# Kernel tuning notes

Measured on AMD Instinct MI355X. Metric: run time of the kernel, lower is better.

Reference implementation:

```python
import jax, jax.numpy as jnp
import numpy as np

WS = (7, 7, 7)          # window size (S, H, W)
NUM_HEADS = 6
DIM = 192
B_, NW = 128, 32        # total windows, windows per image (mask dim)
N = WS[0] * WS[1] * WS[2]  # 343 tokens per window


def _relative_position_index():
    # Faithful replica of the torch __init__ logic (incl. indexing='xy' and
    # the 3*W1-1 / 2*W1-1 multipliers).
    cs = np.arange(WS[0]); ch = np.arange(WS[1]); cw = np.arange(WS[2])
    coords = np.stack(np.meshgrid(cs, ch, cw, indexing='xy'))  # (3, Wh, Ws, Ww)
    cf = coords.reshape(3, -1)                                  # (3, N)
    rel = cf[:, :, None] - cf[:, None, :]                       # (3, N, N)
    rel = rel.transpose(1, 2, 0).astype(np.int64)               # (N, N, 3)
    rel[:, :, 0] += WS[0] - 1
    rel[:, :, 1] += WS[1] - 1
    rel[:, :, 2] += WS[2] - 1
    rel[:, :, 0] *= 3 * WS[1] - 1
    rel[:, :, 1] *= 2 * WS[1] - 1
    return rel.sum(-1)                                          # (N, N) int


def setup_inputs() -> dict:
    key = jax.random.key(0)
    ks = jax.random.split(key, 6)
    C = DIM
    x = jax.random.normal(ks[0], (B_, N, C), dtype=jnp.float32)
    mask = jax.random.normal(ks[1], (NW, N, N), dtype=jnp.float32)
    qkv_w = jax.random.normal(ks[2], (3 * C, C), dtype=jnp.float32) * 0.02
    qkv_b = jnp.zeros((3 * C,), dtype=jnp.float32)
    proj_w = jax.random.normal(ks[3], (C, C), dtype=jnp.float32) * 0.02
    proj_b = jnp.zeros((C,), dtype=jnp.float32)
    table_len = (2 * WS[0] - 1) * (2 * WS[1] - 1) * (2 * WS[2] - 1)
    rpb_table = jax.random.normal(ks[4], (table_len, NUM_HEADS), dtype=jnp.float32) * 0.02
    rel_index = jnp.asarray(_relative_position_index(), dtype=jnp.int32)
    return {"x": x, "mask": mask, "qkv_w": qkv_w, "qkv_b": qkv_b,
            "proj_w": proj_w, "proj_b": proj_b, "rpb_table": rpb_table,
            "rel_index": rel_index}


def reference(x, mask, qkv_w, qkv_b, proj_w, proj_b, rpb_table, rel_index):
    B, n, C = x.shape
    H = NUM_HEADS
    hd = C // H
    scale = hd ** (-0.5)
    qkv = x @ qkv_w.T + qkv_b                      # (B, N, 3C)
    qkv = qkv.reshape(B, n, 3, H, hd).transpose(2, 0, 3, 1, 4)  # (3, B, H, N, hd)
    q, k, v = qkv[0] * scale, qkv[1], qkv[2]
    attn = jnp.einsum('bhnd,bhmd->bhnm', q, k)     # (B, H, N, N)
    bias = rpb_table[rel_index.reshape(-1)].reshape(n, n, H)
    attn = attn + bias.transpose(2, 0, 1)[None]    # (B, H, N, N)
    nW = mask.shape[0]
    attn = attn.reshape(B // nW, nW, H, n, n) + mask[None, :, None]
    attn = jax.nn.softmax(attn.reshape(B, H, n, n), axis=-1)
    out = jnp.einsum('bhnm,bhmd->bhnd', attn, v)   # (B, H, N, hd)
    out = out.transpose(0, 2, 1, 3).reshape(B, n, C)
    return out @ proj_w.T + proj_b
```

## Files before the change

### kernel.cpp

```cpp
#include <hip/hip_runtime.h>
#include <hip/hip_fp16.h>
#include <hip/hip_bf16.h>
#include <stdint.h>

#define WN 343
#define NH 6
#define HD 32
#define CD 192
#define NB 128
#define NWM 32
#define BMROW 352
#define BMSLICE (11*16*BMROW)

typedef __attribute__((ext_vector_type(8))) short short8;
typedef __attribute__((ext_vector_type(4))) float f32x4;

__device__ __forceinline__ unsigned short f2bf(float f) {
  union { float f; uint32_t u; } v; v.f = f;
  uint32_t r = v.u + 0x7fffu + ((v.u >> 16) & 1u);
  return (unsigned short)(r >> 16);
}

__device__ __forceinline__ uint32_t pk2bf(float a, float b) {
  __hip_bfloat162 h = __float22bfloat162_rn(make_float2(a, b));
  return *(uint32_t*)&h;
}

__global__ __launch_bounds__(256) void prep_kernel(
    const float* __restrict__ wq, const float* __restrict__ wp,
    unsigned short* __restrict__ wqb, unsigned short* __restrict__ wpb,
    const int* __restrict__ rel, const float* __restrict__ rpb,
    const float* __restrict__ mask, uint32_t* __restrict__ bP,
    uint32_t* __restrict__ mP) {
  __shared__ float M[352][33];
  const int bid = blockIdx.x;
  if (bid < 66 + 352) {
    const bool isBias = (bid < 66);
    const int sub = isBias ? bid : bid - 66;
    const int grp = sub / 11;
    const int kc = sub - grp * 11;
    const int k0 = kc * 32;
    const float* mw = mask + (size_t)grp * (WN * WN);
    for (int idx = threadIdx.x; idx < 352 * 32; idx += 256) {
      int n = idx >> 5, k = idx & 31;
      float v;
      if (isBias) {
        int nc = (n < WN) ? n : (WN - 1);
        v = (k0 + k < WN) ? rpb[rel[nc * WN + k0 + k] * NH + grp] : -60000.0f;
      } else {
        v = (n < WN && k0 + k < WN) ? mw[n * WN + k0 + k] : 0.0f;
      }
      M[n][k] = v;
    }
    __syncthreads();
    uint32_t* outp = (isBias ? bP : mP) + (size_t)grp * BMSLICE + kc * 16 * BMROW;
#pragma unroll
    for (int rr = 0; rr < 16; ++rr) {
      int kkA = (rr >> 2) * 8 + (rr & 3);
#pragma unroll
      for (int j = 0; j < 2; ++j) {
        int n = threadIdx.x + 256 * j;
        if (n < 352) {
          __half2 hv; hv.x = __float2half(M[n][kkA]); hv.y = __float2half(M[n][kkA + 4]);
          outp[rr * BMROW + n] = *(uint32_t*)&hv;
        }
      }
    }
    return;
  }
  const int NWQ = 3 * CD * CD;
  const int NWP = CD * CD;
  int i4 = ((bid - 418) * 256 + threadIdx.x) * 4;
  const float* src; unsigned short* dst; int off;
  if (i4 < NWQ) { src = wq; dst = wqb; off = i4; }
  else if (i4 < NWQ + NWP) { src = wp; dst = wpb; off = i4 - NWQ; }
  else return;
  f32x4 v = *(const f32x4*)(src + off);
  union { uint2 u2; uint32_t d[2]; } o;
  o.d[0] = pk2bf(v[0], v[1]);
  o.d[1] = pk2bf(v[2], v[3]);
  *(uint2*)(dst + off) = o.u2;
}

__global__ __launch_bounds__(256) void qkv_kernel(
    const float* __restrict__ x, const unsigned short* __restrict__ wqb,
    const float* __restrict__ bvec,
    unsigned short* __restrict__ qb, unsigned short* __restrict__ kb,
    unsigned short* __restrict__ vb) {
  __shared__ __align__(16) unsigned short Xs[128][40];
  __shared__ __align__(16) unsigned short Ws[192][40];
  const int tid = threadIdx.x;
  const int wave = tid >> 6, lane = tid & 63;
  const int quad = lane >> 4, c = lane & 15;
  const int m0 = blockIdx.x * 128;
  const int s = blockIdx.y;
  const int n0 = s * 192;

  f32x4 acc[2][12];
#pragma unroll
  for (int i = 0; i < 2; ++i)
#pragma unroll
    for (int j = 0; j < 12; ++j) acc[i][j] = (f32x4){0.f, 0.f, 0.f, 0.f};

  for (int kt = 0; kt < 6; ++kt) {
    const int k0 = kt * 32;
#pragma unroll
    for (int it = 0; it < 2; ++it) {
      int tq = tid + it * 256;
      int r = tq >> 2, ch = tq & 3;
      const float* src = x + (size_t)(m0 + r) * CD + k0 + ch * 8;
      f32x4 a = *(const f32x4*)src;
      f32x4 b = *(const f32x4*)(src + 4);
      union { short8 v8; uint32_t d[4]; } pk;
      pk.d[0] = pk2bf(a[0], a[1]);
      pk.d[1] = pk2bf(a[2], a[3]);
      pk.d[2] = pk2bf(b[0], b[1]);
      pk.d[3] = pk2bf(b[2], b[3]);
      *(short8*)&Xs[r][ch * 8] = pk.v8;
    }
#pragma unroll
    for (int it = 0; it < 3; ++it) {
      int r = it * 64 + (tid >> 2), ch = tid & 3;
      *(short8*)&Ws[r][ch * 8] =
          *(const short8*)(wqb + (size_t)(n0 + r) * CD + k0 + ch * 8);
    }
    __syncthreads();
    short8 af0 = *(const short8*)&Xs[wave * 32 + c][quad * 8];
    short8 af1 = *(const short8*)&Xs[wave * 32 + 16 + c][quad * 8];
#pragma unroll
    for (int j = 0; j < 12; ++j) {
      short8 bfr = *(const short8*)&Ws[j * 16 + c][quad * 8];
      acc[0][j] = __builtin_amdgcn_mfma_f32_16x16x32_bf16(af0, bfr, acc[0][j], 0, 0, 0);
      acc[1][j] = __builtin_amdgcn_mfma_f32_16x16x32_bf16(af1, bfr, acc[1][j], 0, 0, 0);
    }
    __syncthreads();
  }

  const float qscale = 0.17677669529663689f;
  unsigned short* dst = (s == 0) ? qb : ((s == 1) ? kb : vb);
  const float scl = (s == 0) ? qscale : 1.0f;
  unsigned short (*Lh0)[40] = (unsigned short (*)[40])&Xs[0][0];
  unsigned short (*Lh1)[40] = (unsigned short (*)[40])&Ws[0][0];
  for (int hh = 0; hh < 3; ++hh) {
    __syncthreads();
#pragma unroll
    for (int jj = 0; jj < 4; ++jj) {
      int j = hh * 4 + jj;
      int hl = jj >> 1;
      int dd = (jj & 1) * 16 + c;
      float bn = bvec[n0 + j * 16 + c];
      unsigned short (*L)[40] = hl ? Lh1 : Lh0;
#pragma unroll
      for (int i = 0; i < 2; ++i)
#pragma unroll
        for (int r = 0; r < 4; ++r) {
          int m = wave * 32 + i * 16 + quad * 4 + r;
          L[m][dd] = f2bf((acc[i][j][r] + bn) * scl);
        }
    }
    __syncthreads();
    const int m = tid & 127;
    const int hl = tid >> 7;
    const int M = m0 + m;
    const int b = M / WN;
    const int tok = M - b * WN;
    const int h = hh * 2 + hl;
    unsigned short (*L)[40] = hl ? Lh1 : Lh0;
    unsigned short* drow = dst + (((size_t)b * NH + h) * WN + tok) * HD;
#pragma unroll
    for (int t2 = 0; t2 < 4; ++t2) {
      int d0 = t2 * 8;
      *(short8*)&drow[d0] = *(const short8*)&L[m][d0];
    }
  }
}

__global__ __launch_bounds__(512) void attn_kernel(
    const unsigned short* __restrict__ qb, const unsigned short* __restrict__ kb,
    const unsigned short* __restrict__ vb, const uint32_t* __restrict__ biasP,
    const uint32_t* __restrict__ maskP, unsigned short* __restrict__ ob) {
  __shared__ __align__(16) unsigned short Ks[352][40];
  __shared__ __align__(16) unsigned short Vt[HD][360];
  const int h = blockIdx.x, b = blockIdx.y;
  const int wdx = b & (NWM - 1);
  const int tid = threadIdx.x;
  const int wave = tid >> 6, lane = tid & 63;
  const int quad = lane >> 4, c = lane & 15;
  const size_t base = ((size_t)b * NH + h) * (WN * HD);
  const unsigned short* q = qb + base;
  const unsigned short* k = kb + base;
  const unsigned short* v = vb + base;
  const uint32_t* bP = biasP + (size_t)h * BMSLICE;
  const uint32_t* mP = maskP + (size_t)wdx * BMSLICE;

  for (int t = tid; t < WN * 4; t += 512) {
    int r = t >> 2, ch = t & 3;
    int kk = r & 31;
    int row = (r & ~31) + 16 * ((kk >> 2) & 1) + 4 * (kk >> 3) + (kk & 3);
    *(short8*)&Ks[row][ch * 8] = *(const short8*)(k + r * HD + ch * 8);
  }
  for (int t = tid; t < 9 * 32; t += 512) {
    int kg = WN + (t >> 5);
    int kk = kg & 31;
    int row = (kg & ~31) + 16 * ((kk >> 2) & 1) + 4 * (kk >> 3) + (kk & 3);
    Ks[row][t & 31] = 0;
  }
  for (int t = tid; t < WN; t += 512) {
#pragma unroll
    for (int ch = 0; ch < 4; ++ch) {
      short8 vv = *(const short8*)(v + t * HD + ch * 8);
#pragma unroll
      for (int j = 0; j < 8; ++j) Vt[ch * 8 + j][t] = vv[j];
    }
  }
  for (int t = tid; t < 9 * 32; t += 512) {
    Vt[t & 31][WN + (t >> 5)] = 0;
  }
  __syncthreads();

  for (int qt = wave; qt < 22; qt += 8) {
    const int q0 = qt * 16;
    int qr = q0 + c; if (qr > WN - 1) qr = WN - 1;
    const short8 qf = *(const short8*)(q + qr * HD + quad * 8);
    const uint32_t* bRow = bP + (size_t)(quad * 4) * BMROW + q0 + c;
    const uint32_t* mRow = mP + (size_t)(quad * 4) * BMROW + q0 + c;

    f32x4 o0 = (f32x4){0.f, 0.f, 0.f, 0.f}, o1 = (f32x4){0.f, 0.f, 0.f, 0.f};
    float l = 0.f;
#pragma unroll
    for (int kc = 0; kc < 11; ++kc) {
      f32x4 cc0, cc1;
#pragma unroll
      for (int r = 0; r < 4; ++r) {
        uint32_t bw = bRow[(kc * 16 + r) * BMROW];
        uint32_t mw = mRow[(kc * 16 + r) * BMROW];
        __half2 s2 = __hadd2(*(__half2*)&bw, *(__half2*)&mw);
        float2 f = __half22float2(s2);
        cc0[r] = f.x;
        cc1[r] = f.y;
      }
      const int k0 = kc * 32;
      short8 kf0 = *(const short8*)&Ks[k0 + c][quad * 8];
      short8 kf1 = *(const short8*)&Ks[k0 + 16 + c][quad * 8];
      f32x4 s0 = __builtin_amdgcn_mfma_f32_16x16x32_bf16(kf0, qf, cc0, 0, 0, 0);
      f32x4 s1 = __builtin_amdgcn_mfma_f32_16x16x32_bf16(kf1, qf, cc1, 0, 0, 0);
      float p0 = __expf(s0[0]), p1 = __expf(s0[1]);
      float p2 = __expf(s0[2]), p3 = __expf(s0[3]);
      float p4 = __expf(s1[0]), p5 = __expf(s1[1]);
      float p6 = __expf(s1[2]), p7 = __expf(s1[3]);
      l += (p0 + p1 + p2 + p3) + (p4 + p5 + p6 + p7);
      union { short8 v8; uint32_t d[4]; } pf;
      pf.d[0] = pk2bf(p0, p1);
      pf.d[1] = pk2bf(p2, p3);
      pf.d[2] = pk2bf(p4, p5);
      pf.d[3] = pk2bf(p6, p7);
      short8 vf0 = *(const short8*)&Vt[c][k0 + quad * 8];
      short8 vf1 = *(const short8*)&Vt[16 + c][k0 + quad * 8];
      o0 = __builtin_amdgcn_mfma_f32_16x16x32_bf16(pf.v8, vf0, o0, 0, 0, 0);
      o1 = __builtin_amdgcn_mfma_f32_16x16x32_bf16(pf.v8, vf1, o1, 0, 0, 0);
    }
    l += __shfl_xor(l, 16);
    l += __shfl_xor(l, 32);

#pragma unroll
    for (int r = 0; r < 4; ++r) {
      int n = q0 + quad * 4 + r;
      if (n < WN) {
        float lq = __shfl(l, quad * 4 + r, 16);
        float inv = 1.0f / lq;
        size_t orow = ((size_t)b * WN + n) * CD + h * HD;
        ob[orow + c] = f2bf(o0[r] * inv);
        ob[orow + 16 + c] = f2bf(o1[r] * inv);
      }
    }
  }
}

__global__ __launch_bounds__(256) void proj_kernel(
    const unsigned short* __restrict__ ob, const unsigned short* __restrict__ wpb,
    const float* __restrict__ bvec, float* __restrict__ out) {
  __shared__ __align__(16) unsigned short Xs[64][40];
  __shared__ __align__(16) unsigned short Ws[192][40];
  const int tid = threadIdx.x;
  const int wave = tid >> 6, lane = tid & 63;
  const int quad = lane >> 4, c = lane & 15;
  const int m0 = blockIdx.x * 64;

  f32x4 acc[12];
#pragma unroll
  for (int j = 0; j < 12; ++j) acc[j] = (f32x4){0.f, 0.f, 0.f, 0.f};

  for (int kt = 0; kt < 6; ++kt) {
    const int k0 = kt * 32;
    {
      int r = tid >> 2, ch = tid & 3;
      *(short8*)&Xs[r][ch * 8] =
          *(const short8*)(ob + (size_t)(m0 + r) * CD + k0 + ch * 8);
    }
#pragma unroll
    for (int it = 0; it < 3; ++it) {
      int r = it * 64 + (tid >> 2), ch = tid & 3;
      *(short8*)&Ws[r][ch * 8] =
          *(const short8*)(wpb + (size_t)r * CD + k0 + ch * 8);
    }
    __syncthreads();
    short8 af = *(const short8*)&Xs[wave * 16 + c][quad * 8];
#pragma unroll
    for (int j = 0; j < 12; ++j) {
      short8 bfr = *(const short8*)&Ws[j * 16 + c][quad * 8];
      acc[j] = __builtin_amdgcn_mfma_f32_16x16x32_bf16(af, bfr, acc[j], 0, 0, 0);
    }
    __syncthreads();
  }

#pragma unroll
  for (int j = 0; j < 12; ++j) {
    int col = j * 16 + c;
    float bn = bvec[col];
#pragma unroll
    for (int r = 0; r < 4; ++r) {
      int m = m0 + wave * 16 + quad * 4 + r;
      out[(size_t)m * CD + col] = acc[j][r] + bn;
    }
  }
}

extern "C" void kernel_launch(void* const* d_in, const int* in_sizes, int n_in,
                              void* d_out, int out_size, void* d_ws, size_t ws_size,
                              hipStream_t stream) {
  const float* x      = (const float*)d_in[0];
  const float* mask   = (const float*)d_in[1];
  const float* qkv_w  = (const float*)d_in[2];
  const float* qkv_b  = (const float*)d_in[3];
  const float* proj_w = (const float*)d_in[4];
  const float* proj_b = (const float*)d_in[5];
  const float* rpb    = (const float*)d_in[6];
  const int*   rel    = (const int*)d_in[7];
  float* out = (float*)d_out;

  char* ws = (char*)d_ws;
  uint32_t* biasP = (uint32_t*)ws;
  size_t off = 1486848;
  uint32_t* maskP = (uint32_t*)(ws + off); off += 7929856;
  unsigned short* qb = (unsigned short*)(ws + off); off += 16859136;
  unsigned short* kb = (unsigned short*)(ws + off); off += 16859136;
  unsigned short* vb = (unsigned short*)(ws + off); off += 16859136;
  unsigned short* obuf = (unsigned short*)(ws + off); off += 16859136;
  unsigned short* wqb = (unsigned short*)(ws + off); off += 221184;
  unsigned short* wpb = (unsigned short*)(ws + off); off += 73728;

  hipLaunchKernelGGL(prep_kernel, dim3(418 + 144), dim3(256), 0, stream,
                     qkv_w, proj_w, wqb, wpb, rel, rpb, mask, biasP, maskP);
  hipLaunchKernelGGL(qkv_kernel, dim3(343, 3), dim3(256), 0, stream,
                     x, wqb, qkv_b, qb, kb, vb);
  hipLaunchKernelGGL(attn_kernel, dim3(NH, NB), dim3(512), 0, stream,
                     qb, kb, vb, biasP, maskP, obuf);
  hipLaunchKernelGGL(proj_kernel, dim3(686), dim3(256), 0, stream,
                     obuf, wpb, proj_b, out);
}
```

Baseline: 224.3 us.

## Fold log2e into scores, repack bias/mask for vector loads, and remap attention blocks

Bias and mask are pre-scaled by log2(e) and the query scale absorbs log2(e), so the softmax can call the hardware exp2 directly instead of __expf. The packed fp16 bias/mask layout is reorganized so each lane fetches its four rows with a single 16-byte load rather than four strided 4-byte loads. The attention grid becomes 1D with a block-index remap meant to group blocks sharing the same mask window and head, likely to improve L2/XCD locality of bias and mask slices. Scaling bias and mask before fp16 conversion slightly changes rounding, and the padding value is adjusted to stay in fp16 range.

```diff
diff --git a/kernel.cpp b/kernel.cpp
--- a/kernel.cpp
+++ b/kernel.cpp
@@ -11,6 +11,8 @@
 #define NWM 32
 #define BMROW 352
 #define BMSLICE (11*16*BMROW)
+#define BMKC (16*BMROW)
+#define LOG2E 1.4426950408889634f
 
 typedef __attribute__((ext_vector_type(8))) short short8;
 typedef __attribute__((ext_vector_type(4))) float f32x4;
@@ -23,6 +25,11 @@
 
 __device__ __forceinline__ uint32_t pk2bf(float a, float b) {
   __hip_bfloat162 h = __float22bfloat162_rn(make_float2(a, b));
+  return *(uint32_t*)&h;
+}
+
+__device__ __forceinline__ uint32_t pkh2(float a, float b) {
+  __half2 h; h.x = __float2half(a); h.y = __float2half(b);
   return *(uint32_t*)&h;
 }
 
@@ -46,23 +53,27 @@
       float v;
       if (isBias) {
         int nc = (n < WN) ? n : (WN - 1);
-        v = (k0 + k < WN) ? rpb[rel[nc * WN + k0 + k] * NH + grp] : -60000.0f;
+        v = (k0 + k < WN) ? rpb[rel[nc * WN + k0 + k] * NH + grp] * LOG2E
+                          : -30000.0f;
       } else {
-        v = (n < WN && k0 + k < WN) ? mw[n * WN + k0 + k] : 0.0f;
+        v = (n < WN && k0 + k < WN) ? mw[n * WN + k0 + k] * LOG2E : 0.0f;
       }
       M[n][k] = v;
     }
     __syncthreads();
-    uint32_t* outp = (isBias ? bP : mP) + (size_t)grp * BMSLICE + kc * 16 * BMROW;
-#pragma unroll
-    for (int rr = 0; rr < 16; ++rr) {
-      int kkA = (rr >> 2) * 8 + (rr & 3);
+    uint32_t* outp = (isBias ? bP : mP) + (size_t)grp * BMSLICE + (size_t)kc * BMKC;
+#pragma unroll
+    for (int quad = 0; quad < 4; ++quad) {
 #pragma unroll
       for (int j = 0; j < 2; ++j) {
         int n = threadIdx.x + 256 * j;
         if (n < 352) {
-          __half2 hv; hv.x = __float2half(M[n][kkA]); hv.y = __float2half(M[n][kkA + 4]);
-          outp[rr * BMROW + n] = *(uint32_t*)&hv;
+          uint4 o;
+          o.x = pkh2(M[n][quad * 8 + 0], M[n][quad * 8 + 4]);
+          o.y = pkh2(M[n][quad * 8 + 1], M[n][quad * 8 + 5]);
+          o.z = pkh2(M[n][quad * 8 + 2], M[n][quad * 8 + 6]);
+          o.w = pkh2(M[n][quad * 8 + 3], M[n][quad * 8 + 7]);
+          *(uint4*)(outp + ((size_t)quad * 352 + n) * 4) = o;
         }
       }
     }
@@ -136,7 +147,7 @@
     __syncthreads();
   }
 
-  const float qscale = 0.17677669529663689f;
+  const float qscale = 0.25503486f;
   unsigned short* dst = (s == 0) ? qb : ((s == 1) ? kb : vb);
   const float scl = (s == 0) ? qscale : 1.0f;
   unsigned short (*Lh0)[40] = (unsigned short (*)[40])&Xs[0][0];
@@ -181,8 +192,12 @@
     const uint32_t* __restrict__ maskP, unsigned short* __restrict__ ob) {
   __shared__ __align__(16) unsigned short Ks[352][40];
   __shared__ __align__(16) unsigned short Vt[HD][360];
-  const int h = blockIdx.x, b = blockIdx.y;
-  const int wdx = b & (NWM - 1);
+  const int bid = blockIdx.x;
+  const int job = (bid & 7) * 96 + (bid >> 3);
+  const int wdx = job / 24;
+  const int inner = job - wdx * 24;
+  const int h = inner >> 2;
+  const int b = (inner & 3) * 32 + wdx;
   const int tid = threadIdx.x;
   const int wave = tid >> 6, lane = tid & 63;
   const int quad = lane >> 4, c = lane & 15;
@@ -222,32 +237,36 @@
     const int q0 = qt * 16;
     int qr = q0 + c; if (qr > WN - 1) qr = WN - 1;
     const short8 qf = *(const short8*)(q + qr * HD + quad * 8);
-    const uint32_t* bRow = bP + (size_t)(quad * 4) * BMROW + q0 + c;
-    const uint32_t* mRow = mP + (size_t)(quad * 4) * BMROW + q0 + c;
+    const uint32_t* bRow = bP + ((size_t)quad * 352 + q0 + c) * 4;
+    const uint32_t* mRow = mP + ((size_t)quad * 352 + q0 + c) * 4;
 
     f32x4 o0 = (f32x4){0.f, 0.f, 0.f, 0.f}, o1 = (f32x4){0.f, 0.f, 0.f, 0.f};
     float l = 0.f;
 #pragma unroll
     for (int kc = 0; kc < 11; ++kc) {
+      uint4 bw4 = *(const uint4*)(bRow + (size_t)kc * BMKC);
+      uint4 mw4 = *(const uint4*)(mRow + (size_t)kc * BMKC);
       f32x4 cc0, cc1;
-#pragma unroll
-      for (int r = 0; r < 4; ++r) {
-        uint32_t bw = bRow[(kc * 16 + r) * BMROW];
-        uint32_t mw = mRow[(kc * 16 + r) * BMROW];
-        __half2 s2 = __hadd2(*(__half2*)&bw, *(__half2*)&mw);
-        float2 f = __half22float2(s2);
-        cc0[r] = f.x;
-        cc1[r] = f.y;
+      {
+        __half2 s2; float2 f;
+        s2 = __hadd2(*(__half2*)&bw4.x, *(__half2*)&mw4.x);
+        f = __half22float2(s2); cc0[0] = f.x; cc1[0] = f.y;
+        s2 = __hadd2(*(__half2*)&bw4.y, *(__half2*)&mw4.y);
+        f = __half22float2(s2); cc0[1] = f.x; cc1[1] = f.y;
+        s2 = __hadd2(*(__half2*)&bw4.z, *(__half2*)&mw4.z);
+        f = __half22float2(s2); cc0[2] = f.x; cc1[2] = f.y;
+        s2 = __hadd2(*(__half2*)&bw4.w, *(__half2*)&mw4.w);
+        f = __half22float2(s2); cc0[3] = f.x; cc1[3] = f.y;
       }
       const int k0 = kc * 32;
       short8 kf0 = *(const short8*)&Ks[k0 + c][quad * 8];
       short8 kf1 = *(const short8*)&Ks[k0 + 16 + c][quad * 8];
       f32x4 s0 = __builtin_amdgcn_mfma_f32_16x16x32_bf16(kf0, qf, cc0, 0, 0, 0);
       f32x4 s1 = __builtin_amdgcn_mfma_f32_16x16x32_bf16(kf1, qf, cc1, 0, 0, 0);
-      float p0 = __expf(s0[0]), p1 = __expf(s0[1]);
-      float p2 = __expf(s0[2]), p3 = __expf(s0[3]);
-      float p4 = __expf(s1[0]), p5 = __expf(s1[1]);
-      float p6 = __expf(s1[2]), p7 = __expf(s1[3]);
+      float p0 = __builtin_amdgcn_exp2f(s0[0]), p1 = __builtin_amdgcn_exp2f(s0[1]);
+      float p2 = __builtin_amdgcn_exp2f(s0[2]), p3 = __builtin_amdgcn_exp2f(s0[3]);
+      float p4 = __builtin_amdgcn_exp2f(s1[0]), p5 = __builtin_amdgcn_exp2f(s1[1]);
+      float p6 = __builtin_amdgcn_exp2f(s1[2]), p7 = __builtin_amdgcn_exp2f(s1[3]);
       l += (p0 + p1 + p2 + p3) + (p4 + p5 + p6 + p7);
       union { short8 v8; uint32_t d[4]; } pf;
       pf.d[0] = pk2bf(p0, p1);
@@ -353,7 +372,7 @@
                      qkv_w, proj_w, wqb, wpb, rel, rpb, mask, biasP, maskP);
   hipLaunchKernelGGL(qkv_kernel, dim3(343, 3), dim3(256), 0, stream,
                      x, wqb, qkv_b, qb, kb, vb);
-  hipLaunchKernelGGL(attn_kernel, dim3(NH, NB), dim3(512), 0, stream,
+  hipLaunchKernelGGL(attn_kernel, dim3(NH * NB), dim3(512), 0, stream,
                      qb, kb, vb, biasP, maskP, obuf);
   hipLaunchKernelGGL(proj_kernel, dim3(686), dim3(256), 0, stream,
                      obuf, wpb, proj_b, out);
```

Measured after the change: 219.8 us. 2.0% less time.
